# Kernel optimization log

Measured on AMD Instinct MI355X. Metric: run time of the kernel, lower is better.

Reference implementation:

```python
import jax, jax.numpy as jnp
import numpy as np

VOCAB = 50257
E = 1024
CTX = 1024
C = 50
NEG = 10


def setup_inputs() -> dict:
    key = jax.random.key(0)
    ks = jax.random.split(key, 10)
    return {
        "x": jax.random.randint(ks[0], (1,), 0, VOCAB),
        "context": jax.random.randint(ks[1], (C,), 0, VOCAB),
        "neg_samples": jax.random.randint(ks[2], (C, NEG), 0, VOCAB),
        "emb": jax.random.normal(ks[3], (VOCAB, E), jnp.float32) * 0.02,
        "M_w": jax.random.normal(ks[4], (CTX, E), jnp.float32) * 0.02,
        "M_b": jnp.zeros((CTX,), jnp.float32),
        "U_w": jax.random.normal(ks[5], (CTX, 2 * CTX), jnp.float32) * 0.02,
        "U_b": jnp.zeros((CTX,), jnp.float32),
        "W_w": jax.random.normal(ks[6], (CTX, 2 * CTX), jnp.float32) * 0.02,
        "W_b": jnp.zeros((CTX,), jnp.float32),
        "prior_mus": jax.random.normal(ks[7], (VOCAB, CTX), jnp.float32) * 0.02,
        # keep sigmas away from 0 so log(sigma^2) is well-behaved
        "prior_sigmas": jax.random.uniform(ks[8], (VOCAB, CTX), jnp.float32, 0.5, 1.5),
    }


def reference(x, context, neg_samples, emb, M_w, M_b, U_w, U_b, W_w, W_b,
              prior_mus, prior_sigmas):
    c_len = context.shape[0]
    # Rw: Embedding(x) [1,E] repeated to [C,E], then M (Linear E->CTX)
    Rw = emb[x] @ M_w.T + M_b                       # [1, CTX]
    Rw = jnp.broadcast_to(Rw, (c_len, Rw.shape[-1]))  # [C, CTX]
    Rc = emb[context] @ M_w.T + M_b                 # [C, CTX]
    h = jax.nn.relu(jnp.concatenate([Rw, Rc], axis=1)).sum(0)  # [2*CTX]
    mu = U_w @ h + U_b                              # [CTX]
    # NOTE: posterior covariance is diag(sigma), NOT diag(sigma^2)
    sigma = jax.nn.softplus(W_w @ h + W_b)          # [CTX]

    k = mu.shape[0]
    log_det_p = jnp.sum(jnp.log(sigma))

    def kl_post_to(m, s2):
        # KL( N(mu, diag(sigma)) || N(m, diag(s2)) ), batched over leading dims
        return 0.5 * (jnp.sum((sigma + (m - mu) ** 2) / s2 + jnp.log(s2), axis=-1)
                      - k - log_det_p)

    kl_pos = kl_post_to(prior_mus[context], prior_sigmas[context] ** 2)        # [C]
    kl_neg = kl_post_to(prior_mus[neg_samples], prior_sigmas[neg_samples] ** 2)  # [C, NEG]
    likelihood = jnp.maximum(0.0, kl_neg - kl_pos[:, None] + 1.0).sum()
    kl_prior = kl_post_to(prior_mus[x], prior_sigmas[x] ** 2)                  # [1]
    return likelihood - kl_prior
```

## Files before the change

kernel.cpp:

```cpp
#include <hip/hip_runtime.h>
#include <math.h>

#define EDIM 1024
#define CTXDIM 1024
#define H2 2048


#define AST(p, v) __hip_atomic_store((p), (v), __ATOMIC_RELAXED, __HIP_MEMORY_SCOPE_AGENT)
#define ALD(p)    __hip_atomic_load((p), __ATOMIC_RELAXED, __HIP_MEMORY_SCOPE_AGENT)

__global__ __launch_bounds__(1024) void k_h(
    const float* __restrict__ emb, const float* __restrict__ Mw,
    const float* __restrict__ Mb, const int* __restrict__ x,
    const int* __restrict__ ctx, int C, float* __restrict__ ws)
{
    __shared__ int   idxs[64];
    __shared__ float pacc[16];
    __shared__ float pxs[4];
    const int tid  = threadIdx.x;
    const int w    = tid >> 6;
    const int lane = tid & 63;
    const int c    = w & 3;
    const int g    = w >> 2;
    const int j    = blockIdx.x * 4 + c;

    if (blockIdx.x == 0) {
        ws[4096 + tid] = 0.f;
        if (tid < 64) ws[5120 + tid] = 0.f;
    }
    if (tid <= C) idxs[tid] = (tid == 0) ? x[0] : ctx[tid - 1];

    const float4* mrow = (const float4*)(Mw + (size_t)j * EDIM);
    const float4 mw0 = mrow[lane];
    const float4 mw1 = mrow[lane + 64];
    const float4 mw2 = mrow[lane + 128];
    const float4 mw3 = mrow[lane + 192];
    const float bj = Mb[j];
    __syncthreads();

    float acc = 0.f, px = 0.f;
#pragma unroll 2
    for (int r = g; r <= C; r += 4) {
        const int idx = idxs[r];
        const float4* e4 = (const float4*)(emb + (size_t)idx * EDIM);
        const float4 a  = e4[lane];
        const float4 bb = e4[lane + 64];
        const float4 d  = e4[lane + 128];
        const float4 e  = e4[lane + 192];
        float s = a.x*mw0.x + a.y*mw0.y + a.z*mw0.z + a.w*mw0.w;
        s += bb.x*mw1.x + bb.y*mw1.y + bb.z*mw1.z + bb.w*mw1.w;
        s += d.x*mw2.x + d.y*mw2.y + d.z*mw2.z + d.w*mw2.w;
        s += e.x*mw3.x + e.y*mw3.y + e.z*mw3.z + e.w*mw3.w;
#pragma unroll
        for (int m = 32; m >= 1; m >>= 1) s += __shfl_xor(s, m);
        const float v = fmaxf(s + bj, 0.f);
        if (r == 0) px = (float)C * v;
        else        acc += v;
    }
    if (lane == 0) {
        pacc[w] = acc;
        if (g == 0) pxs[c] = px;
    }
    __syncthreads();
    if (tid < 4) {
        const int jj = blockIdx.x * 4 + tid;
        ws[jj]          = pxs[tid];
        ws[CTXDIM + jj] = pacc[tid] + pacc[tid + 4] + pacc[tid + 8] + pacc[tid + 12];
    }
}

__global__ __launch_bounds__(512) void k_tail(
    const float* __restrict__ Uw, const float* __restrict__ Ub,
    const float* __restrict__ Ww, const float* __restrict__ Wb,
    const float* __restrict__ pmu, const float* __restrict__ psig,
    const int* __restrict__ x, const int* __restrict__ ctx,
    const int* __restrict__ negs, int C, int CN, int NEG, int KDIM,
    int nsblk, float* __restrict__ ws, float* __restrict__ out)
{
    __shared__ float smem[2048];
    __shared__ int   winflag;
    const int tid  = threadIdx.x;
    const int w    = tid >> 6;
    const int lane = tid & 63;
    const int b    = blockIdx.x;
    unsigned* bar  = (unsigned*)(ws + 4096);
    float* Sbuf    = ws + 5248;

    if (b < 256) {
        float4* hbuf = (float4*)smem;
        hbuf[tid] = ((const float4*)ws)[tid];
        __syncthreads();

        const int W = b * 8 + w;
        const bool is_mu = (W < CTXDIM);
        const int rr = W & (CTXDIM - 1);
        const float4* Wr4 = (const float4*)((is_mu ? Uw : Ww) + (size_t)rr * H2);
        float s = 0.f;
#pragma unroll
        for (int k = 0; k < 8; ++k) {
            const float4 wv = Wr4[lane + 64 * k];
            const float4 hv = hbuf[lane + 64 * k];
            s += wv.x*hv.x + wv.y*hv.y + wv.z*hv.z + wv.w*hv.w;
        }
#pragma unroll
        for (int m = 32; m >= 1; m >>= 1) s += __shfl_xor(s, m);
        if (lane == 0) {
            if (is_mu) {
                AST(&ws[2048 + rr], s + Ub[rr]);
            } else {
                const float v = s + Wb[rr];
                AST(&ws[3072 + rr], fmaxf(v, 0.f) + log1pf(expf(-fabsf(v))));
            }
        }
        __syncthreads();
        if (tid == 0) {
            const unsigned old = __hip_atomic_fetch_add(&bar[32 * (b & 15)], 1u,
                                   __ATOMIC_RELAXED, __HIP_MEMORY_SCOPE_AGENT);
            if (old == 15u) {
                const unsigned o2 = __hip_atomic_fetch_add(&bar[32 * 16], 1u,
                                      __ATOMIC_RELAXED, __HIP_MEMORY_SCOPE_AGENT);
                if (o2 == 15u) {
#pragma unroll
                    for (int i = 0; i < 16; ++i)
                        AST(&bar[32 * (17 + i)], 1u);
                }
            }
        }
        return;
    }

    const int t = (b - 256) * 8 + w;
    const int ntask = 2 + C + CN;

    const bool iskl = (t >= 1 && t < ntask);
    float4 gm[4], gsv[4];
    if (iskl) {
        int idx;
        if (t == 1)          idx = x[0];
        else if (t < 2 + C)  idx = ctx[t - 2];
        else                 idx = negs[t - 2 - C];
        const float4* m4 = (const float4*)(pmu  + (size_t)idx * CTXDIM);
        const float4* s4 = (const float4*)(psig + (size_t)idx * CTXDIM);
#pragma unroll
        for (int k = 0; k < 4; ++k) {
            gm[k]  = m4[lane + 64 * k];
            gsv[k] = s4[lane + 64 * k];
        }
    }

    if (tid == 0) {
        while (ALD(&bar[32 * (17 + (b & 15))]) == 0u)
            __builtin_amdgcn_s_sleep(8);
    }
    __syncthreads();
    __builtin_amdgcn_sched_barrier(0);

    {
        const unsigned long long* src = (const unsigned long long*)(ws + 2048);
#pragma unroll
        for (int q = 0; q < 2; ++q) {
            const int i = tid + 512 * q;
            const unsigned long long v = __hip_atomic_load(&src[i],
                __ATOMIC_RELAXED, __HIP_MEMORY_SCOPE_AGENT);
            smem[2 * i]     = __uint_as_float((unsigned)(v & 0xffffffffu));
            smem[2 * i + 1] = __uint_as_float((unsigned)(v >> 32));
        }
    }
    __syncthreads();

    {
        float acc = 0.f;
        if (t == 0) {
#pragma unroll
            for (int k = 0; k < 16; ++k) acc += logf(smem[1024 + lane + 64 * k]);
        } else {
            const float4* ms4 = (const float4*)smem;
#pragma unroll
            for (int k = 0; k < 4; ++k) {
                const int i = lane + 64 * k;
                const float4 m  = gm[k];
                const float4 sv = gsv[k];
                const float4 mu = ms4[i];
                const float4 sg = ms4[256 + i];
                { const float s2 = sv.x*sv.x; const float dd = m.x-mu.x; acc += (sg.x + dd*dd)/s2 + logf(s2); }
                { const float s2 = sv.y*sv.y; const float dd = m.y-mu.y; acc += (sg.y + dd*dd)/s2 + logf(s2); }
                { const float s2 = sv.z*sv.z; const float dd = m.z-mu.z; acc += (sg.z + dd*dd)/s2 + logf(s2); }
                { const float s2 = sv.w*sv.w; const float dd = m.w-mu.w; acc += (sg.w + dd*dd)/s2 + logf(s2); }
            }
        }
#pragma unroll
        for (int m = 32; m >= 1; m >>= 1) acc += __shfl_xor(acc, m);
        if (lane == 0) AST(&Sbuf[t], acc);
    }

    __syncthreads();
    if (w == 0) {
        __builtin_amdgcn_fence(__ATOMIC_RELEASE, "agent");
        int win = 0;
        if (lane == 0) {
            const unsigned old = __hip_atomic_fetch_add(&bar[32 * 33], 1u,
                                   __ATOMIC_RELAXED, __HIP_MEMORY_SCOPE_AGENT);
            win = (old == (unsigned)(nsblk - 1));
        }
        win = __shfl(win, 0);
        if (win) {
            __builtin_amdgcn_fence(__ATOMIC_ACQUIRE, "agent");
            float lik = 0.f;
            for (int i = lane; i < CN; i += 64) {
                const float sn = ALD(&Sbuf[2 + C + i]);
                const float sp = ALD(&Sbuf[2 + i / NEG]);
                lik += fmaxf(0.f, 0.5f * (sn - sp) + 1.0f);
            }
#pragma unroll
            for (int m = 32; m >= 1; m >>= 1) lik += __shfl_xor(lik, m);
            if (lane == 0) {
                const float ld = ALD(&Sbuf[0]);
                const float sx = ALD(&Sbuf[1]);
                out[0] = lik - 0.5f * (sx - (float)KDIM - ld);
            }
        }
    }
}

extern "C" void kernel_launch(void* const* d_in, const int* in_sizes, int n_in,
                              void* d_out, int out_size, void* d_ws, size_t ws_size,
                              hipStream_t stream) {
    const int*   x    = (const int*)d_in[0];
    const int*   ctx  = (const int*)d_in[1];
    const int*   negs = (const int*)d_in[2];
    const float* emb  = (const float*)d_in[3];
    const float* Mw   = (const float*)d_in[4];
    const float* Mb   = (const float*)d_in[5];
    const float* Uw   = (const float*)d_in[6];
    const float* Ub   = (const float*)d_in[7];
    const float* Ww   = (const float*)d_in[8];
    const float* Wb   = (const float*)d_in[9];
    const float* pmu  = (const float*)d_in[10];
    const float* psig = (const float*)d_in[11];
    float* ws  = (float*)d_ws;
    float* out = (float*)d_out;

    const int C    = in_sizes[1];
    const int CN   = in_sizes[2];
    const int NEG  = CN / C;
    const int KDIM = in_sizes[5];

    const int ntask = 2 + C + CN;
    const int nsblk = (ntask + 7) / 8;

    k_h<<<CTXDIM / 4, 1024, 0, stream>>>(emb, Mw, Mb, x, ctx, C, ws);
    k_tail<<<256 + nsblk, 512, 0, stream>>>(Uw, Ub, Ww, Wb, pmu, psig,
                                            x, ctx, negs, C, CN, NEG, KDIM,
                                            nsblk, ws, out);
}
```

Baseline: 25.89 us.

## Fuse h, mu/sigma and KL stages into one persistent kernel with flag barriers

Merges the two launches into a single kernel with three block roles: h computation, mu/sigma GEMV, and KL scoring. The roles synchronise through hierarchical atomic counters and flags in the workspace. The GEMV blocks now prefetch their U/W rows into registers before waiting on the h flag, so weight loads overlap the first stage. The barrier reset moves to a hipMemsetAsync, which adds a memset node to the stream. The design relies on all blocks being co-resident, since spinning blocks wait on producer blocks.

```diff
diff --git a/kernel.cpp b/kernel.cpp
--- a/kernel.cpp
+++ b/kernel.cpp
@@ -4,132 +4,160 @@
 #define EDIM 1024
 #define CTXDIM 1024
 #define H2 2048
+#define NH 512
+#define NMS 256
 
 
 #define AST(p, v) __hip_atomic_store((p), (v), __ATOMIC_RELAXED, __HIP_MEMORY_SCOPE_AGENT)
 #define ALD(p)    __hip_atomic_load((p), __ATOMIC_RELAXED, __HIP_MEMORY_SCOPE_AGENT)
 
-__global__ __launch_bounds__(1024) void k_h(
+__global__ __launch_bounds__(512) void k_all(
     const float* __restrict__ emb, const float* __restrict__ Mw,
-    const float* __restrict__ Mb, const int* __restrict__ x,
-    const int* __restrict__ ctx, int C, float* __restrict__ ws)
-{
-    __shared__ int   idxs[64];
-    __shared__ float pacc[16];
-    __shared__ float pxs[4];
-    const int tid  = threadIdx.x;
-    const int w    = tid >> 6;
-    const int lane = tid & 63;
-    const int c    = w & 3;
-    const int g    = w >> 2;
-    const int j    = blockIdx.x * 4 + c;
-
-    if (blockIdx.x == 0) {
-        ws[4096 + tid] = 0.f;
-        if (tid < 64) ws[5120 + tid] = 0.f;
-    }
-    if (tid <= C) idxs[tid] = (tid == 0) ? x[0] : ctx[tid - 1];
-
-    const float4* mrow = (const float4*)(Mw + (size_t)j * EDIM);
-    const float4 mw0 = mrow[lane];
-    const float4 mw1 = mrow[lane + 64];
-    const float4 mw2 = mrow[lane + 128];
-    const float4 mw3 = mrow[lane + 192];
-    const float bj = Mb[j];
-    __syncthreads();
-
-    float acc = 0.f, px = 0.f;
-#pragma unroll 2
-    for (int r = g; r <= C; r += 4) {
-        const int idx = idxs[r];
-        const float4* e4 = (const float4*)(emb + (size_t)idx * EDIM);
-        const float4 a  = e4[lane];
-        const float4 bb = e4[lane + 64];
-        const float4 d  = e4[lane + 128];
-        const float4 e  = e4[lane + 192];
-        float s = a.x*mw0.x + a.y*mw0.y + a.z*mw0.z + a.w*mw0.w;
-        s += bb.x*mw1.x + bb.y*mw1.y + bb.z*mw1.z + bb.w*mw1.w;
-        s += d.x*mw2.x + d.y*mw2.y + d.z*mw2.z + d.w*mw2.w;
-        s += e.x*mw3.x + e.y*mw3.y + e.z*mw3.z + e.w*mw3.w;
-#pragma unroll
-        for (int m = 32; m >= 1; m >>= 1) s += __shfl_xor(s, m);
-        const float v = fmaxf(s + bj, 0.f);
-        if (r == 0) px = (float)C * v;
-        else        acc += v;
-    }
-    if (lane == 0) {
-        pacc[w] = acc;
-        if (g == 0) pxs[c] = px;
-    }
-    __syncthreads();
-    if (tid < 4) {
-        const int jj = blockIdx.x * 4 + tid;
-        ws[jj]          = pxs[tid];
-        ws[CTXDIM + jj] = pacc[tid] + pacc[tid + 4] + pacc[tid + 8] + pacc[tid + 12];
-    }
-}
-
-__global__ __launch_bounds__(512) void k_tail(
-    const float* __restrict__ Uw, const float* __restrict__ Ub,
-    const float* __restrict__ Ww, const float* __restrict__ Wb,
-    const float* __restrict__ pmu, const float* __restrict__ psig,
-    const int* __restrict__ x, const int* __restrict__ ctx,
-    const int* __restrict__ negs, int C, int CN, int NEG, int KDIM,
-    int nsblk, float* __restrict__ ws, float* __restrict__ out)
+    const float* __restrict__ Mb, const float* __restrict__ Uw,
+    const float* __restrict__ Ub, const float* __restrict__ Ww,
+    const float* __restrict__ Wb, const float* __restrict__ pmu,
+    const float* __restrict__ psig, const int* __restrict__ x,
+    const int* __restrict__ ctx, const int* __restrict__ negs,
+    int C, int CN, int NEG, int KDIM, int nsblk,
+    float* __restrict__ ws, float* __restrict__ out)
 {
     __shared__ float smem[2048];
-    __shared__ int   winflag;
+    __shared__ int   idxs[64];
+    __shared__ float pacc[8];
+    __shared__ float pxs[2];
     const int tid  = threadIdx.x;
     const int w    = tid >> 6;
     const int lane = tid & 63;
     const int b    = blockIdx.x;
     unsigned* bar  = (unsigned*)(ws + 4096);
-    float* Sbuf    = ws + 5248;
-
-    if (b < 256) {
-        float4* hbuf = (float4*)smem;
-        hbuf[tid] = ((const float4*)ws)[tid];
-        __syncthreads();
-
-        const int W = b * 8 + w;
+    float* Sbuf    = ws + 6272;
+
+    if (b < NH) {
+        if (tid <= C) idxs[tid] = (tid == 0) ? x[0] : ctx[tid - 1];
+        const int c = w & 1;
+        const int g = w >> 1;
+        const int j = b * 2 + c;
+        const float4* mrow = (const float4*)(Mw + (size_t)j * EDIM);
+        const float4 mw0 = mrow[lane];
+        const float4 mw1 = mrow[lane + 64];
+        const float4 mw2 = mrow[lane + 128];
+        const float4 mw3 = mrow[lane + 192];
+        const float bj = Mb[j];
+        __syncthreads();
+
+        float acc = 0.f, px = 0.f;
+#pragma unroll 2
+        for (int r = g; r <= C; r += 4) {
+            const int idx = idxs[r];
+            const float4* e4 = (const float4*)(emb + (size_t)idx * EDIM);
+            const float4 a  = e4[lane];
+            const float4 bb = e4[lane + 64];
+            const float4 d  = e4[lane + 128];
+            const float4 e  = e4[lane + 192];
+            float s = a.x*mw0.x + a.y*mw0.y + a.z*mw0.z + a.w*mw0.w;
+            s += bb.x*mw1.x + bb.y*mw1.y + bb.z*mw1.z + bb.w*mw1.w;
+            s += d.x*mw2.x + d.y*mw2.y + d.z*mw2.z + d.w*mw2.w;
+            s += e.x*mw3.x + e.y*mw3.y + e.z*mw3.z + e.w*mw3.w;
+#pragma unroll
+            for (int m = 32; m >= 1; m >>= 1) s += __shfl_xor(s, m);
+            const float v = fmaxf(s + bj, 0.f);
+            if (r == 0) px = (float)C * v;
+            else        acc += v;
+        }
+        if (lane == 0) {
+            pacc[w] = acc;
+            if (g == 0) pxs[c] = px;
+        }
+        __syncthreads();
+        if (tid < 2) {
+            const int jj = b * 2 + tid;
+            AST(&ws[jj], pxs[tid]);
+            AST(&ws[CTXDIM + jj],
+                pacc[tid] + pacc[tid + 2] + pacc[tid + 4] + pacc[tid + 6]);
+        }
+        __syncthreads();
+        if (tid == 0) {
+            const unsigned old = __hip_atomic_fetch_add(&bar[32 * (b & 15)], 1u,
+                                   __ATOMIC_RELAXED, __HIP_MEMORY_SCOPE_AGENT);
+            if (old == 31u) {
+                const unsigned o2 = __hip_atomic_fetch_add(&bar[32 * 16], 1u,
+                                      __ATOMIC_RELAXED, __HIP_MEMORY_SCOPE_AGENT);
+                if (o2 == 15u) {
+#pragma unroll
+                    for (int i = 0; i < 16; ++i) AST(&bar[32 * (17 + i)], 1u);
+                }
+            }
+        }
+        return;
+    }
+
+    if (b < NH + NMS) {
+        const int mb = b - NH;
+        const int W = mb * 8 + w;
         const bool is_mu = (W < CTXDIM);
         const int rr = W & (CTXDIM - 1);
         const float4* Wr4 = (const float4*)((is_mu ? Uw : Ww) + (size_t)rr * H2);
+
+        float4 wv[8];
+#pragma unroll
+        for (int k = 0; k < 8; ++k) wv[k] = Wr4[lane + 64 * k];
+        const float bias = is_mu ? Ub[rr] : Wb[rr];
+
+        if (tid == 0) {
+            while (ALD(&bar[32 * (17 + (mb & 15))]) == 0u)
+                __builtin_amdgcn_s_sleep(8);
+        }
+        __syncthreads();
+        __builtin_amdgcn_sched_barrier(0);
+
+        {
+            const unsigned long long* src = (const unsigned long long*)ws;
+#pragma unroll
+            for (int q = 0; q < 2; ++q) {
+                const int i = tid + 512 * q;
+                const unsigned long long v = __hip_atomic_load(&src[i],
+                    __ATOMIC_RELAXED, __HIP_MEMORY_SCOPE_AGENT);
+                smem[2 * i]     = __uint_as_float((unsigned)(v & 0xffffffffu));
+                smem[2 * i + 1] = __uint_as_float((unsigned)(v >> 32));
+            }
+        }
+        __syncthreads();
+
+        const float4* h4 = (const float4*)smem;
         float s = 0.f;
 #pragma unroll
         for (int k = 0; k < 8; ++k) {
-            const float4 wv = Wr4[lane + 64 * k];
-            const float4 hv = hbuf[lane + 64 * k];
-            s += wv.x*hv.x + wv.y*hv.y + wv.z*hv.z + wv.w*hv.w;
+            const float4 hv = h4[lane + 64 * k];
+            s += wv[k].x*hv.x + wv[k].y*hv.y + wv[k].z*hv.z + wv[k].w*hv.w;
         }
 #pragma unroll
         for (int m = 32; m >= 1; m >>= 1) s += __shfl_xor(s, m);
         if (lane == 0) {
             if (is_mu) {
-                AST(&ws[2048 + rr], s + Ub[rr]);
+                AST(&ws[2048 + rr], s + bias);
             } else {
-                const float v = s + Wb[rr];
+                const float v = s + bias;
                 AST(&ws[3072 + rr], fmaxf(v, 0.f) + log1pf(expf(-fabsf(v))));
             }
         }
         __syncthreads();
         if (tid == 0) {
-            const unsigned old = __hip_atomic_fetch_add(&bar[32 * (b & 15)], 1u,
+            const unsigned old = __hip_atomic_fetch_add(&bar[32 * (33 + (mb & 15))], 1u,
                                    __ATOMIC_RELAXED, __HIP_MEMORY_SCOPE_AGENT);
             if (old == 15u) {
-                const unsigned o2 = __hip_atomic_fetch_add(&bar[32 * 16], 1u,
+                const unsigned o2 = __hip_atomic_fetch_add(&bar[32 * 49], 1u,
                                       __ATOMIC_RELAXED, __HIP_MEMORY_SCOPE_AGENT);
                 if (o2 == 15u) {
 #pragma unroll
-                    for (int i = 0; i < 16; ++i)
-                        AST(&bar[32 * (17 + i)], 1u);
+                    for (int i = 0; i < 16; ++i) AST(&bar[32 * (50 + i)], 1u);
                 }
             }
         }
         return;
     }
 
-    const int t = (b - 256) * 8 + w;
+    const int sc = b - NH - NMS;
+    const int t = sc * 8 + w;
     const int ntask = 2 + C + CN;
 
     const bool iskl = (t >= 1 && t < ntask);
@@ -149,7 +177,7 @@
     }
 
     if (tid == 0) {
-        while (ALD(&bar[32 * (17 + (b & 15))]) == 0u)
+        while (ALD(&bar[32 * (50 + (sc & 15))]) == 0u)
             __builtin_amdgcn_s_sleep(8);
     }
     __syncthreads();
@@ -198,7 +226,7 @@
         __builtin_amdgcn_fence(__ATOMIC_RELEASE, "agent");
         int win = 0;
         if (lane == 0) {
-            const unsigned old = __hip_atomic_fetch_add(&bar[32 * 33], 1u,
+            const unsigned old = __hip_atomic_fetch_add(&bar[32 * 66], 1u,
                                    __ATOMIC_RELAXED, __HIP_MEMORY_SCOPE_AGENT);
             win = (old == (unsigned)(nsblk - 1));
         }
@@ -248,8 +276,8 @@
     const int ntask = 2 + C + CN;
     const int nsblk = (ntask + 7) / 8;
 
-    k_h<<<CTXDIM / 4, 1024, 0, stream>>>(emb, Mw, Mb, x, ctx, C, ws);
-    k_tail<<<256 + nsblk, 512, 0, stream>>>(Uw, Ub, Ww, Wb, pmu, psig,
-                                            x, ctx, negs, C, CN, NEG, KDIM,
-                                            nsblk, ws, out);
+    (void)hipMemsetAsync((char*)d_ws + 4096 * sizeof(float), 0, 67 * 128, stream);
+    k_all<<<NH + NMS + nsblk, 512, 0, stream>>>(emb, Mw, Mb, Uw, Ub, Ww, Wb,
+                                                pmu, psig, x, ctx, negs,
+                                                C, CN, NEG, KDIM, nsblk, ws, out);
 }
```

Result: slower. 31.84 us (+23.0%).
